# Performance work log

Measured on AMD Instinct MI355X. Metric: run time of the kernel, lower is better.

The kernel has to match this reference:

```python
import jax, jax.numpy as jnp
import numpy as np

H = 64  # hidden size
T = 11  # unrolled timesteps


def setup_inputs() -> dict:
    key = jax.random.key(0)
    ks = jax.random.split(key, 8)
    B, V, E = 65536, 50000, 100
    return {
        "sent": jax.random.randint(ks[0], (B, T), 0, V, dtype=jnp.int32),
        "emb_W": jax.random.normal(ks[1], (V, E), jnp.float32) * 0.05,
        "W_ih": jax.random.normal(ks[2], (4 * H, E), jnp.float32) * 0.05,
        "W_hh": jax.random.normal(ks[3], (4 * H, H), jnp.float32) * 0.05,
        "b_ih": jax.random.normal(ks[4], (4 * H,), jnp.float32) * 0.05,
        "b_hh": jax.random.normal(ks[5], (4 * H,), jnp.float32) * 0.05,
        "fc_W": jax.random.normal(ks[6], (14, H), jnp.float32) * 0.05,
        "fc_b": jax.random.normal(ks[7], (14,), jnp.float32) * 0.05,
    }


def _lstm_cell(x, h, c, W_ih, W_hh, b_ih, b_hh):
    # gates order in torch LSTMCell: i, f, g, o
    gates = x @ W_ih.T + b_ih + h @ W_hh.T + b_hh  # [B, 4H]
    i, f, g, o = jnp.split(gates, 4, axis=-1)
    c_new = jax.nn.sigmoid(f) * c + jax.nn.sigmoid(i) * jnp.tanh(g)
    h_new = jax.nn.sigmoid(o) * jnp.tanh(c_new)
    return h_new, c_new


def reference(sent, emb_W, W_ih, W_hh, b_ih, b_hh, fc_W, fc_b):
    embed = emb_W[sent]  # [B, T, E]
    B = embed.shape[0]
    h0 = jnp.zeros((B, H), embed.dtype)
    c0 = jnp.zeros((B, H), embed.dtype)
    xs = jnp.swapaxes(embed[:, :T, :], 0, 1)  # [T, B, E]

    def step(carry, x):
        h, c = carry
        h, c = _lstm_cell(x, h, c, W_ih, W_hh, b_ih, b_hh)
        return (h, c), None

    (h_last, _), _ = jax.lax.scan(step, (h0, c0), xs)
    logits = h_last @ fc_W.T + fc_b  # [B, 14]
    return jax.nn.log_softmax(logits, axis=-1)
```

## Files before the change

### kernel.cpp

```cpp
#include <hip/hip_runtime.h>
#include <hip/hip_bf16.h>

#define T_STEPS 11
#define E_DIM   100
#define XSL     2048
#define NDMA    (2 * T_STEPS)

typedef int   i32x4   __attribute__((ext_vector_type(4)));
typedef float f32x4   __attribute__((ext_vector_type(4)));
typedef _Float16 h16x2 __attribute__((ext_vector_type(2)));
typedef _Float16 h16x4 __attribute__((ext_vector_type(4)));
typedef _Float16 h16x8 __attribute__((ext_vector_type(8)));

typedef __attribute__((address_space(1))) const unsigned int g_as1;
typedef __attribute__((address_space(3))) unsigned int l_as3;

__device__ __forceinline__ h16x2 spl2(float v) {
    _Float16 h = (_Float16)v;
    return (h16x2){h, h};
}
__device__ __forceinline__ h16x2 pk2(float a, float b) {
    return __builtin_bit_cast(h16x2, __builtin_amdgcn_cvt_pkrtz(a, b));
}
__device__ __forceinline__ unsigned char f2fp8(float f) {
    return (unsigned char)(__builtin_amdgcn_cvt_pk_fp8_f32(f, 0.f, 0, false) & 0xff);
}
__device__ __forceinline__ long long ll_lo(i32x4 v) {
    return ((long long)(unsigned)v[1] << 32) | (unsigned)v[0];
}
__device__ __forceinline__ long long ll_hi(i32x4 v) {
    return ((long long)(unsigned)v[3] << 32) | (unsigned)v[2];
}

__device__ __forceinline__ h16x2 tanh5(h16x2 x) {
    h16x2 x2 = x * x;
    h16x2 p = x2 * spl2(0.13333333f) + spl2(-0.33333333f);
    p = x2 * p + spl2(1.0f);
    return x * p;
}
__device__ __forceinline__ h16x2 tanh7(h16x2 x) {
    h16x2 x2 = x * x;
    h16x2 p = x2 * spl2(-0.05396825f) + spl2(0.13333333f);
    p = x2 * p + spl2(-0.33333333f);
    p = x2 * p + spl2(1.0f);
    return x * p;
}
__device__ __forceinline__ h16x2 sig3(h16x2 x) {
    h16x2 x2 = x * x;
    h16x2 p = x2 * spl2(-0.020833334f) + spl2(0.25f);
    return x * p + spl2(0.5f);
}

__global__ void pack_all(const float* __restrict__ emb,
                         const float* __restrict__ W_ih, const float* __restrict__ W_hh,
                         const float* __restrict__ b_ih, const float* __restrict__ b_hh,
                         unsigned char* __restrict__ embp8, unsigned char* __restrict__ Wx8,
                         unsigned char* __restrict__ Wh8, float* __restrict__ biasf, int V)
{
    int b = blockIdx.x;
    int tid = threadIdx.x;
    if (b < 128) {
        int id = b * 256 + tid;
        int n = id >> 7, k = id & 127;
        float v = (k < E_DIM) ? W_ih[n * E_DIM + k] : 0.f;
        int kt = k >> 5;
        int lane = (n & 15) | (((k & 31) >> 3) << 4);
        Wx8[((kt * 16 + (n >> 4)) * 64 + lane) * 8 + (k & 7)] = f2fp8(v);
    } else if (b < 192) {
        int id = (b - 128) * 256 + tid;
        int n = id >> 6, k = id & 63;
        int kt = k >> 5;
        int lane = (n & 15) | (((k & 31) >> 3) << 4);
        Wh8[((kt * 16 + (n >> 4)) * 64 + lane) * 8 + (k & 7)] = f2fp8(W_hh[n * 64 + k]);
    } else if (b == 192) {
        biasf[tid] = b_ih[tid] + b_hh[tid];
    } else {
        int id = (b - 193) * 256 + tid;
        if (id >= V * 8) return;
        int row = id >> 3;
        int c8 = id & 7;
        int p = c8 >> 2, qq = c8 & 3;
        const float* xr = emb + (size_t)row * E_DIM;
        float v[16];
        #pragma unroll
        for (int w = 0; w < 16; ++w) {
            int k = p * 64 + (w >> 3) * 32 + qq * 8 + (w & 7);
            v[w] = (k < E_DIM) ? xr[k] : 0.f;
        }
        int4 o;
        int* op = &o.x;
        #pragma unroll
        for (int w = 0; w < 4; ++w) {
            int d = __builtin_amdgcn_cvt_pk_fp8_f32(v[w*4+0], v[w*4+1], 0, false);
            d = __builtin_amdgcn_cvt_pk_fp8_f32(v[w*4+2], v[w*4+3], d, true);
            op[w] = d;
        }
        *reinterpret_cast<int4*>(embp8 + (size_t)row * 128 + c8 * 16) = o;
    }
}

template<int PACKED>
__global__ __launch_bounds__(256, 4)
void lstm_fused(const int* __restrict__ sent,
                const float* __restrict__ emb, const unsigned char* __restrict__ embp8,
                const unsigned char* __restrict__ Wx8, const unsigned char* __restrict__ Wh8,
                const float* __restrict__ biasf,
                const float* __restrict__ fc_W, const float* __restrict__ fc_b,
                float* __restrict__ out)
{
    __shared__ unsigned char xlds[T_STEPS * XSL];
    __shared__ unsigned char hlds[2][1024];
    __shared__ float biaslds[256];
    __shared__ short hscr[16 * 68];
    const int tid  = threadIdx.x;
    const int wv   = tid >> 6;
    const int lane = tid & 63;
    const int r    = lane & 15;
    const int q    = lane >> 4;
    const int b0   = blockIdx.x * 16;

    for (int d = wv; d < NDMA; d += 4) {
        int sl = d >> 1, half = d & 1;
        int c  = half * 4 + (lane >> 4);
        int rr = lane & 15;
        int idx = sent[(b0 + rr) * T_STEPS + sl];
        if (PACKED) {
            const unsigned char* src = embp8 + (size_t)idx * 128 + c * 16;
            __builtin_amdgcn_global_load_lds(
                (g_as1*)src, (l_as3*)&xlds[sl * XSL + half * 1024], 16, 0, 0);
        } else {
            const float* xr = emb + (size_t)idx * E_DIM;
            int p = c >> 2, qq = c & 3;
            float v[16];
            #pragma unroll
            for (int w = 0; w < 16; ++w) {
                int k = p * 64 + (w >> 3) * 32 + qq * 8 + (w & 7);
                v[w] = (k < E_DIM) ? xr[k] : 0.f;
            }
            int4 o;
            int* op = &o.x;
            #pragma unroll
            for (int w = 0; w < 4; ++w) {
                int dd = __builtin_amdgcn_cvt_pk_fp8_f32(v[w*4+0], v[w*4+1], 0, false);
                dd = __builtin_amdgcn_cvt_pk_fp8_f32(v[w*4+2], v[w*4+3], dd, true);
                op[w] = dd;
            }
            *reinterpret_cast<int4*>(&xlds[sl * XSL + (half * 64 + lane) * 16]) = o;
        }
    }

    long long wx[4][4], wh[2][4];
    #pragma unroll
    for (int kt = 0; kt < 4; ++kt)
        #pragma unroll
        for (int g = 0; g < 4; ++g)
            wx[kt][g] = *reinterpret_cast<const long long*>(
                Wx8 + ((kt * 16 + g * 4 + wv) * 64 + lane) * 8);
    #pragma unroll
    for (int kt = 0; kt < 2; ++kt)
        #pragma unroll
        for (int g = 0; g < 4; ++g)
            wh[kt][g] = *reinterpret_cast<const long long*>(
                Wh8 + ((kt * 16 + g * 4 + wv) * 64 + lane) * 8);
    #pragma unroll
    for (int kt = 0; kt < 4; ++kt)
        #pragma unroll
        for (int g = 0; g < 4; ++g)
            asm volatile("" : "+v"(wx[kt][g]));
    #pragma unroll
    for (int kt = 0; kt < 2; ++kt)
        #pragma unroll
        for (int g = 0; g < 4; ++g)
            asm volatile("" : "+v"(wh[kt][g]));

    biaslds[tid] = biasf[tid];
    reinterpret_cast<int*>(&hlds[0][0])[tid] = 0;

    __builtin_amdgcn_s_waitcnt(0);
    __syncthreads();

    auto acc_bias_x = [&](int sl, f32x4* acc) {
        #pragma unroll
        for (int g = 0; g < 4; ++g)
            acc[g] = *reinterpret_cast<const f32x4*>(
                &biaslds[(g * 4 + wv) * 16 + q * 4]);
        #pragma unroll
        for (int p = 0; p < 2; ++p) {
            i32x4 v = *reinterpret_cast<const i32x4*>(
                &xlds[sl * XSL + ((p * 4 + q) * 16 + r) * 16]);
            long long lo = ll_lo(v), hi = ll_hi(v);
            #pragma unroll
            for (int g = 0; g < 4; ++g)
                acc[g] = __builtin_amdgcn_mfma_f32_16x16x32_fp8_fp8(wx[2*p][g], lo, acc[g], 0, 0, 0);
            #pragma unroll
            for (int g = 0; g < 4; ++g)
                acc[g] = __builtin_amdgcn_mfma_f32_16x16x32_fp8_fp8(wx[2*p+1][g], hi, acc[g], 0, 0, 0);
        }
    };

    h16x2 c01 = spl2(0.f), c23 = spl2(0.f);
    f32x4 acc[4];
    acc_bias_x(0, acc);

    const int hq  = (wv & 1) * 2 + (q >> 1);
    const int hoff = (hq * 16 + r) * 16 + (wv >> 1) * 8 + (q & 1) * 4;

    #pragma unroll
    for (int t = 0; t < T_STEPS; ++t) {
        i32x4 hv = *reinterpret_cast<const i32x4*>(&hlds[t & 1][(q * 16 + r) * 16]);
        long long bh0 = ll_lo(hv), bh1 = ll_hi(hv);
        #pragma unroll
        for (int g = 0; g < 4; ++g)
            acc[g] = __builtin_amdgcn_mfma_f32_16x16x32_fp8_fp8(wh[0][g], bh0, acc[g], 0, 0, 0);
        #pragma unroll
        for (int g = 0; g < 4; ++g)
            acc[g] = __builtin_amdgcn_mfma_f32_16x16x32_fp8_fp8(wh[1][g], bh1, acc[g], 0, 0, 0);

        h16x2 gi0 = pk2(acc[0][0], acc[0][1]), gi1 = pk2(acc[0][2], acc[0][3]);
        h16x2 gf0 = pk2(acc[1][0], acc[1][1]), gf1 = pk2(acc[1][2], acc[1][3]);
        h16x2 gg0 = pk2(acc[2][0], acc[2][1]), gg1 = pk2(acc[2][2], acc[2][3]);
        h16x2 go0 = pk2(acc[3][0], acc[3][1]), go1 = pk2(acc[3][2], acc[3][3]);
        c01 = sig3(gf0) * c01 + sig3(gi0) * tanh5(gg0);
        c23 = sig3(gf1) * c23 + sig3(gi1) * tanh5(gg1);
        h16x2 h01 = sig3(go0) * tanh7(c01);
        h16x2 h23 = sig3(go1) * tanh7(c23);

        int hw = __builtin_amdgcn_cvt_pk_fp8_f32((float)h01[0], (float)h01[1], 0, false);
        hw = __builtin_amdgcn_cvt_pk_fp8_f32((float)h23[0], (float)h23[1], hw, true);
        *reinterpret_cast<int*>(&hlds[(t + 1) & 1][hoff]) = hw;

        if (t == T_STEPS - 1) {
            h16x4 hn = { h01[0], h01[1], h23[0], h23[1] };
            *reinterpret_cast<h16x4*>(&hscr[r * 68 + wv * 16 + q * 4]) = hn;
        }

        if (t + 1 < T_STEPS) acc_bias_x(t + 1, acc);

        __syncthreads();
    }

    const int row_local = wv * 4 + q;
    const int cls = r;
    const int brow = b0 + row_local;
    float s = (cls < 14) ? fc_b[cls] : 0.f;
    const float* wrow = fc_W + ((cls < 14) ? cls : 0) * 64;
    #pragma unroll
    for (int ch = 0; ch < 8; ++ch) {
        h16x8 hv8 = *reinterpret_cast<const h16x8*>(&hscr[row_local * 68 + ch * 8]);
        #pragma unroll
        for (int j = 0; j < 8; ++j)
            s = fmaf((float)hv8[j], wrow[ch * 8 + j], s);
    }
    float lg = (cls < 14) ? s : -1e30f;
    float mx = lg;
    mx = fmaxf(mx, __shfl_xor(mx, 1));
    mx = fmaxf(mx, __shfl_xor(mx, 2));
    mx = fmaxf(mx, __shfl_xor(mx, 4));
    mx = fmaxf(mx, __shfl_xor(mx, 8));
    float se = __expf(lg - mx);
    se += __shfl_xor(se, 1);
    se += __shfl_xor(se, 2);
    se += __shfl_xor(se, 4);
    se += __shfl_xor(se, 8);
    float lse = mx + __logf(se);
    if (cls < 14) out[(size_t)brow * 14 + cls] = lg - lse;
}

extern "C" void kernel_launch(void* const* d_in, const int* in_sizes, int n_in,
                              void* d_out, int out_size, void* d_ws, size_t ws_size,
                              hipStream_t stream)
{
    const int*   sent = (const int*)d_in[0];
    const float* emb  = (const float*)d_in[1];
    const float* W_ih = (const float*)d_in[2];
    const float* W_hh = (const float*)d_in[3];
    const float* b_ih = (const float*)d_in[4];
    const float* b_hh = (const float*)d_in[5];
    const float* fc_W = (const float*)d_in[6];
    const float* fc_b = (const float*)d_in[7];
    float* out = (float*)d_out;

    const int B = in_sizes[0] / T_STEPS;
    const int V = in_sizes[1] / E_DIM;
    const size_t emb_bytes = (size_t)V * 128;
    const size_t need = emb_bytes + 32768 + 16384 + 1024;
    const bool packed = ws_size >= need;

    unsigned char* embp8 = (unsigned char*)d_ws;
    unsigned char* Wx8   = embp8 + emb_bytes;
    unsigned char* Wh8   = Wx8 + 32768;
    float*         biasf = (float*)(Wh8 + 16384);
    if (!packed) {
        Wx8   = (unsigned char*)d_ws;
        Wh8   = Wx8 + 32768;
        biasf = (float*)(Wh8 + 16384);
        embp8 = nullptr;
    }

    const int grid = B / 16;
    if (packed) {
        int pgrid = 193 + (V * 8 + 255) / 256;
        pack_all<<<pgrid, 256, 0, stream>>>(emb, W_ih, W_hh, b_ih, b_hh,
                                            embp8, Wx8, Wh8, biasf, V);
        lstm_fused<1><<<grid, 256, 0, stream>>>(sent, emb, embp8, Wx8, Wh8,
                                                biasf, fc_W, fc_b, out);
    } else {
        pack_all<<<193, 256, 0, stream>>>(emb, W_ih, W_hh, b_ih, b_hh,
                                          nullptr, Wx8, Wh8, biasf, 0);
        lstm_fused<0><<<grid, 256, 0, stream>>>(sent, emb, nullptr, Wx8, Wh8,
                                                biasf, fc_W, fc_b, out);
    }
}
```

Measured before the change: 148.8 us.

## Use 16x16x128 scaled FP8 MFMA for input projection with repacked layouts

Repacks the W_ih and embedding FP8 layouts so each lane holds 32 contiguous K values. The input projection then uses the MI355X 16x16x128 f8f6f4 scaled MFMA (one instruction per gate group instead of four 16x16x32 ones), with unit scales. This cuts MFMA issue count and register moves. It also raises wave priority around the recurrent critical section so the h-dependent chain is scheduled ahead of other waves' input projections.

```diff
diff --git a/kernel.cpp b/kernel.cpp
--- a/kernel.cpp
+++ b/kernel.cpp
@@ -7,6 +7,7 @@
 #define NDMA    (2 * T_STEPS)
 
 typedef int   i32x4   __attribute__((ext_vector_type(4)));
+typedef int   i32x8   __attribute__((ext_vector_type(8)));
 typedef float f32x4   __attribute__((ext_vector_type(4)));
 typedef _Float16 h16x2 __attribute__((ext_vector_type(2)));
 typedef _Float16 h16x4 __attribute__((ext_vector_type(4)));
@@ -63,9 +64,9 @@
         int id = b * 256 + tid;
         int n = id >> 7, k = id & 127;
         float v = (k < E_DIM) ? W_ih[n * E_DIM + k] : 0.f;
-        int kt = k >> 5;
-        int lane = (n & 15) | (((k & 31) >> 3) << 4);
-        Wx8[((kt * 16 + (n >> 4)) * 64 + lane) * 8 + (k & 7)] = f2fp8(v);
+        int mt = n >> 4;
+        int lane = (n & 15) | ((k >> 5) << 4);
+        Wx8[(mt * 64 + lane) * 32 + (k & 31)] = f2fp8(v);
     } else if (b < 192) {
         int id = (b - 128) * 256 + tid;
         int n = id >> 6, k = id & 63;
@@ -79,12 +80,11 @@
         if (id >= V * 8) return;
         int row = id >> 3;
         int c8 = id & 7;
-        int p = c8 >> 2, qq = c8 & 3;
         const float* xr = emb + (size_t)row * E_DIM;
         float v[16];
         #pragma unroll
         for (int w = 0; w < 16; ++w) {
-            int k = p * 64 + (w >> 3) * 32 + qq * 8 + (w & 7);
+            int k = c8 * 16 + w;
             v[w] = (k < E_DIM) ? xr[k] : 0.f;
         }
         int4 o;
@@ -130,11 +130,10 @@
                 (g_as1*)src, (l_as3*)&xlds[sl * XSL + half * 1024], 16, 0, 0);
         } else {
             const float* xr = emb + (size_t)idx * E_DIM;
-            int p = c >> 2, qq = c & 3;
             float v[16];
             #pragma unroll
             for (int w = 0; w < 16; ++w) {
-                int k = p * 64 + (w >> 3) * 32 + qq * 8 + (w & 7);
+                int k = c * 16 + w;
                 v[w] = (k < E_DIM) ? xr[k] : 0.f;
             }
             int4 o;
@@ -145,17 +144,16 @@
                 dd = __builtin_amdgcn_cvt_pk_fp8_f32(v[w*4+2], v[w*4+3], dd, true);
                 op[w] = dd;
             }
-            *reinterpret_cast<int4*>(&xlds[sl * XSL + (half * 64 + lane) * 16]) = o;
+            *reinterpret_cast<int4*>(&xlds[sl * XSL + (c * 16 + rr) * 16]) = o;
         }
     }
 
-    long long wx[4][4], wh[2][4];
-    #pragma unroll
-    for (int kt = 0; kt < 4; ++kt)
-        #pragma unroll
-        for (int g = 0; g < 4; ++g)
-            wx[kt][g] = *reinterpret_cast<const long long*>(
-                Wx8 + ((kt * 16 + g * 4 + wv) * 64 + lane) * 8);
+    i32x8 wx[4];
+    #pragma unroll
+    for (int g = 0; g < 4; ++g)
+        wx[g] = *reinterpret_cast<const i32x8*>(
+            Wx8 + ((g * 4 + wv) * 64 + lane) * 32);
+    long long wh[2][4];
     #pragma unroll
     for (int kt = 0; kt < 2; ++kt)
         #pragma unroll
@@ -163,10 +161,8 @@
             wh[kt][g] = *reinterpret_cast<const long long*>(
                 Wh8 + ((kt * 16 + g * 4 + wv) * 64 + lane) * 8);
     #pragma unroll
-    for (int kt = 0; kt < 4; ++kt)
-        #pragma unroll
-        for (int g = 0; g < 4; ++g)
-            asm volatile("" : "+v"(wx[kt][g]));
+    for (int g = 0; g < 4; ++g)
+        asm volatile("" : "+v"(wx[g]));
     #pragma unroll
     for (int kt = 0; kt < 2; ++kt)
         #pragma unroll
@@ -184,18 +180,15 @@
         for (int g = 0; g < 4; ++g)
             acc[g] = *reinterpret_cast<const f32x4*>(
                 &biaslds[(g * 4 + wv) * 16 + q * 4]);
-        #pragma unroll
-        for (int p = 0; p < 2; ++p) {
-            i32x4 v = *reinterpret_cast<const i32x4*>(
-                &xlds[sl * XSL + ((p * 4 + q) * 16 + r) * 16]);
-            long long lo = ll_lo(v), hi = ll_hi(v);
-            #pragma unroll
-            for (int g = 0; g < 4; ++g)
-                acc[g] = __builtin_amdgcn_mfma_f32_16x16x32_fp8_fp8(wx[2*p][g], lo, acc[g], 0, 0, 0);
-            #pragma unroll
-            for (int g = 0; g < 4; ++g)
-                acc[g] = __builtin_amdgcn_mfma_f32_16x16x32_fp8_fp8(wx[2*p+1][g], hi, acc[g], 0, 0, 0);
-        }
+        i32x4 lo = *reinterpret_cast<const i32x4*>(
+            &xlds[sl * XSL + ((2 * q) * 16 + r) * 16]);
+        i32x4 hi = *reinterpret_cast<const i32x4*>(
+            &xlds[sl * XSL + ((2 * q + 1) * 16 + r) * 16]);
+        i32x8 bx = { lo[0], lo[1], lo[2], lo[3], hi[0], hi[1], hi[2], hi[3] };
+        #pragma unroll
+        for (int g = 0; g < 4; ++g)
+            acc[g] = __builtin_amdgcn_mfma_scale_f32_16x16x128_f8f6f4(
+                wx[g], bx, acc[g], 0, 0, 0, 127, 0, 127);
     };
 
     h16x2 c01 = spl2(0.f), c23 = spl2(0.f);
@@ -207,6 +200,7 @@
 
     #pragma unroll
     for (int t = 0; t < T_STEPS; ++t) {
+        __builtin_amdgcn_s_setprio(1);
         i32x4 hv = *reinterpret_cast<const i32x4*>(&hlds[t & 1][(q * 16 + r) * 16]);
         long long bh0 = ll_lo(hv), bh1 = ll_hi(hv);
         #pragma unroll
@@ -228,6 +222,7 @@
         int hw = __builtin_amdgcn_cvt_pk_fp8_f32((float)h01[0], (float)h01[1], 0, false);
         hw = __builtin_amdgcn_cvt_pk_fp8_f32((float)h23[0], (float)h23[1], hw, true);
         *reinterpret_cast<int*>(&hlds[(t + 1) & 1][hoff]) = hw;
+        __builtin_amdgcn_s_setprio(0);
 
         if (t == T_STEPS - 1) {
             h16x4 hn = { h01[0], h01[1], h23[0], h23[1] };
```

New measurement: 151.1 us. No clear change (+1.6%).
